# Optimization experiments

Hardware: AMD Instinct MI355X
Metric: run time of the kernel (lower is better)

Reference implementation:

```python
import jax, jax.numpy as jnp
import numpy as np

# dims
B, T, HID = 2, 2048, 2048
HK, HV, DK, DV, KW = 16, 32, 128, 128, 4
KEY_DIM = HK * DK          # 2048
VAL_DIM = HV * DV          # 4096
CONV_DIM = 2 * KEY_DIM + VAL_DIM  # 8192
EPS = 1e-6


def setup_inputs() -> dict:
    key = jax.random.key(0)
    ks = jax.random.split(key, 10)
    s = 0.02
    return {
        "x": jax.random.normal(ks[0], (B, T, HID), jnp.float32),
        "input_pos": jnp.arange(T, dtype=jnp.int64),
        "W_qkv": jax.random.normal(ks[1], (CONV_DIM, HID), jnp.float32) * s,
        "W_z": jax.random.normal(ks[2], (VAL_DIM, HID), jnp.float32) * s,
        "W_b": jax.random.normal(ks[3], (HV, HID), jnp.float32) * s,
        "W_a": jax.random.normal(ks[4], (HV, HID), jnp.float32) * s,
        "conv_w": jax.random.normal(ks[5], (CONV_DIM, 1, KW), jnp.float32) * 0.2,
        "dt_bias": jnp.ones((HV,), jnp.float32),
        "A_log": jnp.log(jax.random.uniform(ks[6], (HV,), jnp.float32, 1e-3, 16.0)),
        "norm_weight": jnp.ones((DV,), jnp.float32),
        "W_out": jax.random.normal(ks[7], (HID, VAL_DIM), jnp.float32) * s,
    }


def _l2norm(t):
    n = jnp.sqrt(jnp.sum(t * t, axis=-1, keepdims=True))
    return t / jnp.maximum(n, 1e-12)


def _gdn_scan(q, k, v, g, beta):
    # per-batch: q,k [T,HV,DK], v [T,HV,DV], g,beta [T,HV]
    scale = DK ** -0.5
    def step(S, inp):  # S: [HV, DK, DV]
        qt, kt, vt, gt, bt = inp
        S = S * jnp.exp(gt)[:, None, None]
        kv = jnp.einsum('hk,hkv->hv', kt, S)
        S = S + jnp.einsum('hk,hv->hkv', kt, bt[:, None] * (vt - kv))
        o = jnp.einsum('hk,hkv->hv', qt * scale, S)
        return S, o
    S0 = jnp.zeros((HV, DK, DV), q.dtype)
    _, o = jax.lax.scan(step, S0, (q, k, v, g, beta))
    return o  # [T, HV, DV]


def reference(x, input_pos, W_qkv, W_z, W_b, W_a, conv_w, dt_bias, A_log, norm_weight, W_out):
    # conv_state / recurrent_state buffers start at zero (and input_pos[0]==0 resets them),
    # so the causal conv reduces to left-padded depthwise conv and the scan starts from S=0.
    mixed_qkv = jnp.einsum('bth,ch->btc', x, W_qkv)                    # [B,T,CONV_DIM]
    z = jnp.einsum('bth,vh->btv', x, W_z).reshape(B, T, HV, DV)
    beta = jax.nn.sigmoid(jnp.einsum('bth,nh->btn', x, W_b))           # [B,T,HV]
    a = jnp.einsum('bth,nh->btn', x, W_a)
    g = -jnp.exp(A_log) * jax.nn.softplus(a + dt_bias)                 # [B,T,HV]

    # causal depthwise conv1d over time
    xc = mixed_qkv.transpose(0, 2, 1)                                  # [B,C,T]
    yc = jax.lax.conv_general_dilated(
        xc, conv_w, window_strides=(1,), padding=[(KW - 1, 0)],
        dimension_numbers=('NCH', 'OIH', 'NCH'), feature_group_count=CONV_DIM)
    qkv = jax.nn.silu(yc).transpose(0, 2, 1)                           # [B,T,C]

    q = qkv[..., :KEY_DIM].reshape(B, T, HK, DK)
    k = qkv[..., KEY_DIM:2 * KEY_DIM].reshape(B, T, HK, DK)
    v = qkv[..., 2 * KEY_DIM:].reshape(B, T, HV, DV)
    q = _l2norm(q)
    k = _l2norm(k)
    rep = HV // HK
    q = jnp.repeat(q, rep, axis=2)                                     # [B,T,HV,DK]
    k = jnp.repeat(k, rep, axis=2)

    o = jax.vmap(_gdn_scan)(q, k, v, g, beta)                          # [B,T,HV,DV]

    # gated RMSNorm: RMSNorm(o) * weight * silu(z)
    of = o.astype(jnp.float32)
    normed = of * jax.lax.rsqrt(jnp.mean(of * of, axis=-1, keepdims=True) + EPS)
    out = (norm_weight * normed) * jax.nn.silu(z.astype(jnp.float32))
    out = out.reshape(B, T, VAL_DIM)
    return jnp.einsum('btv,hv->bth', out, W_out)
```

## Files before the change

### kernel.cpp

```cpp
#include <hip/hip_runtime.h>

#define BB 2
#define TT 2048
#define HID 2048
#define HK 16
#define HV 32
#define DK 128
#define DV 128
#define KW 4
#define KEY_DIM 2048
#define VAL_DIM 4096
#define CONV_DIM 8192
#define N1PAD 12544
#define M_ROWS 4096
#define CC 64

typedef __attribute__((ext_vector_type(8))) short short8;
typedef __attribute__((ext_vector_type(8))) unsigned short ushort8;
typedef __attribute__((ext_vector_type(4))) float f32x4;

__device__ __forceinline__ unsigned short f2bf(float f) {
  union { float f; unsigned int u; } v; v.f = f;
  unsigned int r = v.u + 0x7FFFu + ((v.u >> 16) & 1u);
  return (unsigned short)(r >> 16);
}
__device__ __forceinline__ float bf2f(unsigned short u) {
  union { unsigned int u; float f; } v; v.u = ((unsigned int)u) << 16; return v.f;
}

template <int CTRL>
__device__ __forceinline__ float dpp_add(float v) {
  union { float f; int i; } a, b;
  a.f = v;
  b.i = __builtin_amdgcn_update_dpp(0, a.i, CTRL, 0xf, 0xf, true);
  return a.f + b.f;
}
template <int CTRL>
__device__ __forceinline__ int dpp_mov(int v) {
  return __builtin_amdgcn_update_dpp(0, v, CTRL, 0xf, 0xf, true);
}
__device__ __forceinline__ float row16_sum(float v) {
  v = dpp_add<0xB1>(v); v = dpp_add<0x4E>(v);
  v = dpp_add<0x141>(v); v = dpp_add<0x140>(v);
  return v;
}
__device__ __forceinline__ float row8_sum(float v) {
  v = dpp_add<0xB1>(v); v = dpp_add<0x4E>(v); v = dpp_add<0x141>(v);
  return v;
}

__device__ __forceinline__ void gload_lds16(const unsigned short* g, unsigned short* l) {
  __builtin_amdgcn_global_load_lds((const __attribute__((address_space(1))) unsigned int*)g,
                                   (__attribute__((address_space(3))) unsigned int*)l,
                                   16, 0, 0);
}
__device__ __forceinline__ void gload_lds4(const float* g, unsigned short* l) {
  __builtin_amdgcn_global_load_lds((const __attribute__((address_space(1))) unsigned int*)g,
                                   (__attribute__((address_space(3))) unsigned int*)l,
                                   4, 0, 0);
}

__device__ __forceinline__ short8 ldswz8(const char* base, int row, int e16) {
  int L = (row << 8) + (e16 << 1);
  return *(const short8*)(base + (L ^ ((row & 7) << 4)));
}
__device__ __forceinline__ short8 ldswz7(const char* base, int row, int e16) {
  int L = (row << 7) + (e16 << 1);
  return *(const short8*)(base + (L ^ ((row & 7) << 4)));
}

__global__ void cvt_bf16(const float* __restrict__ in, unsigned short* __restrict__ out) {
  long i = ((long)blockIdx.x * 256 + threadIdx.x) * 4;
  float4 v = *(const float4*)&in[i];
  unsigned long long p = (unsigned long long)f2bf(v.x)
                       | ((unsigned long long)f2bf(v.y) << 16)
                       | ((unsigned long long)f2bf(v.z) << 32)
                       | ((unsigned long long)f2bf(v.w) << 48);
  *(unsigned long long*)&out[i] = p;
}

__global__ void build_wcat(const float* __restrict__ wqkv, const float* __restrict__ wz,
                           const float* __restrict__ wb, const float* __restrict__ wa,
                           unsigned short* __restrict__ wcat) {
  long idx = (long)blockIdx.x * 256 + threadIdx.x;
  long e = idx * 4;
  long r = e >> 11;
  int cc = (int)(e & 2047);
  unsigned long long p = 0ULL;
  if (r < 12352) {
    const float* src;
    if (r < 8192)       src = wqkv + r * 2048;
    else if (r < 12288) src = wz + (r - 8192) * 2048;
    else if (r < 12320) src = wb + (r - 12288) * 2048;
    else                src = wa + (r - 12320) * 2048;
    float4 v = *(const float4*)&src[cc];
    p = (unsigned long long)f2bf(v.x)
      | ((unsigned long long)f2bf(v.y) << 16)
      | ((unsigned long long)f2bf(v.z) << 32)
      | ((unsigned long long)f2bf(v.w) << 48);
  }
  *(unsigned long long*)&wcat[e] = p;
}

__device__ __forceinline__ void stage256(const unsigned short* __restrict__ G, long rb, int K,
                                         int kt, char* region, int r, int tid, int wid) {
  int i = r * 512 + tid;
  int row = i >> 3;
  int D = i << 4;
  int eb = (D ^ ((row & 7) << 4)) & 127;
  const unsigned short* src = G + (rb + row) * (long)K + kt * 64 + (eb >> 1);
  gload_lds16(src, (unsigned short*)region + r * 4096 + wid * 512);
}

__global__ __launch_bounds__(512, 2) void gemm256(const unsigned short* __restrict__ A,
                                                  const unsigned short* __restrict__ Bw,
                                                  unsigned short* __restrict__ Cout,
                                                  int N, int K) {
  extern __shared__ char gs[];
  const int tid = threadIdx.x, wid = tid >> 6, lane = tid & 63;
  const int lr = lane & 15, lq = lane >> 4;
  const long m0 = (long)blockIdx.y << 8;
  const long n0 = (long)blockIdx.x << 8;
  const int wr = wid >> 2, wc = wid & 3;
  const int nkt = K >> 6;

  f32x4 acc[8][4] = {};

#pragma unroll
  for (int r = 0; r < 4; ++r) {
    stage256(A, m0, K, 0, gs, r, tid, wid);
    stage256(Bw, n0, K, 0, gs + 32768, r, tid, wid);
  }
  asm volatile("s_waitcnt vmcnt(0)" ::: "memory");
  __syncthreads();

  for (int kt = 0; kt < nkt; ++kt) {
    char* cur = gs + ((kt & 1) << 16);
    char* nxt = gs + (((kt + 1) & 1) << 16);
    const char* cA = cur;
    const char* cB = cur + 32768;
    const bool pf = (kt + 1 < nkt);
    short8 bf[2][4];
#pragma unroll
    for (int p = 0; p < 4; ++p) {
      if (pf) {
        stage256(A, m0, K, kt + 1, nxt, p, tid, wid);
        stage256(Bw, n0, K, kt + 1, nxt + 32768, p, tid, wid);
      }
      if (p == 0) {
#pragma unroll
        for (int ks = 0; ks < 2; ++ks)
#pragma unroll
          for (int cf = 0; cf < 4; ++cf)
            bf[ks][cf] = ldswz7(cB, wc * 64 + cf * 16 + lr, ks * 32 + lq * 8);
      }
      short8 af[2][2];
#pragma unroll
      for (int ks = 0; ks < 2; ++ks)
#pragma unroll
        for (int rr = 0; rr < 2; ++rr)
          af[ks][rr] = ldswz7(cA, wr * 128 + (p * 2 + rr) * 16 + lr, ks * 32 + lq * 8);
      __builtin_amdgcn_s_setprio(1);
#pragma unroll
      for (int ks = 0; ks < 2; ++ks)
#pragma unroll
        for (int rr = 0; rr < 2; ++rr)
#pragma unroll
          for (int cf = 0; cf < 4; ++cf)
            acc[p * 2 + rr][cf] = __builtin_amdgcn_mfma_f32_16x16x32_bf16(
                af[ks][rr], bf[ks][cf], acc[p * 2 + rr][cf], 0, 0, 0);
      __builtin_amdgcn_s_setprio(0);
    }
    asm volatile("s_waitcnt vmcnt(0)" ::: "memory");
    __syncthreads();
  }

  const long rbase = m0 + wr * 128 + lq * 4;
  const long cbase = n0 + wc * 64 + lr;
#pragma unroll
  for (int rf = 0; rf < 8; ++rf)
#pragma unroll
    for (int cf = 0; cf < 4; ++cf)
#pragma unroll
      for (int j = 0; j < 4; ++j)
        Cout[(rbase + rf * 16 + j) * N + cbase + cf * 16] = f2bf(acc[rf][cf][j]);
}

template <bool BF16OUT>
__global__ __launch_bounds__(256) void gemm_bt(const unsigned short* __restrict__ A,
                                               const unsigned short* __restrict__ Bw,
                                               void* __restrict__ Cout,
                                               int N, int K) {
  __shared__ unsigned short lds[8192];
  const int tid = threadIdx.x;
  const int wid = tid >> 6;
  const int lane = tid & 63;
  const int m0 = blockIdx.y << 7;
  const int n0 = blockIdx.x << 7;
  const int wr = wid >> 1, wc = wid & 1;

  f32x4 acc[4][4] = {};

  const int srow = (wid << 4) + (lane >> 2);
  const int scol = (lane & 3) << 3;
  const unsigned short* gA0 = A + (long)(m0 + srow) * K + scol;
  const unsigned short* gA1 = A + (long)(m0 + 64 + srow) * K + scol;
  const unsigned short* gB0 = Bw + (long)(n0 + srow) * K + scol;
  const unsigned short* gB1 = Bw + (long)(n0 + 64 + srow) * K + scol;
  unsigned short* ldsA = &lds[wid << 9];
  unsigned short* ldsB = &lds[4096 + (wid << 9)];

  const int lrow = lane & 15;
  const int lk = (lane >> 4) << 3;

  for (int k0 = 0; k0 < K; k0 += 32) {
    __syncthreads();
    gload_lds16(gA0 + k0, ldsA);
    gload_lds16(gA1 + k0, ldsA + 2048);
    gload_lds16(gB0 + k0, ldsB);
    gload_lds16(gB1 + k0, ldsB + 2048);
    __syncthreads();
    short8 av[4], bv[4];
#pragma unroll
    for (int i = 0; i < 4; ++i) {
      av[i] = *(const short8*)&lds[((wr << 6) + (i << 4) + lrow) * 32 + lk];
      bv[i] = *(const short8*)&lds[4096 + ((wc << 6) + (i << 4) + lrow) * 32 + lk];
    }
#pragma unroll
    for (int i = 0; i < 4; ++i)
#pragma unroll
      for (int j = 0; j < 4; ++j)
        acc[i][j] = __builtin_amdgcn_mfma_f32_16x16x32_bf16(av[i], bv[j], acc[i][j], 0, 0, 0);
  }
  const int rbase = m0 + (wr << 6) + ((lane >> 4) << 2);
  const int cbase = n0 + (wc << 6) + (lane & 15);
#pragma unroll
  for (int i = 0; i < 4; ++i)
#pragma unroll
    for (int j = 0; j < 4; ++j)
#pragma unroll
      for (int r = 0; r < 4; ++r) {
        long idx = (long)(rbase + (i << 4) + r) * N + cbase + (j << 4);
        if (BF16OUT) ((unsigned short*)Cout)[idx] = f2bf(acc[i][j][r]);
        else         ((float*)Cout)[idx] = acc[i][j][r];
      }
}

__global__ __launch_bounds__(256) void conv_silu(const unsigned short* __restrict__ C1,
                                                 const float* __restrict__ convw,
                                                 unsigned short* __restrict__ qb,
                                                 unsigned short* __restrict__ kb,
                                                 unsigned short* __restrict__ vb) {
  const int bid = blockIdx.x;
  const int cb = bid & 3, tblk = (bid >> 2) & 63, b = bid >> 8;
  const int c0 = cb * 2048 + threadIdx.x * 8;
  float w0[8], w1[8], w2[8], w3[8];
#pragma unroll
  for (int j = 0; j < 8; ++j) {
    float4 wv = *(const float4*)&convw[(c0 + j) * 4];
    w0[j] = wv.x; w1[j] = wv.y; w2[j] = wv.z; w3[j] = wv.w;
  }
  const int t0 = tblk * 32;
  const long rowbase = ((long)b * TT) * N1PAD + c0;
  float x0[8], x1[8], x2[8];
#pragma unroll
  for (int j = 0; j < 8; ++j) { x0[j] = 0.f; x1[j] = 0.f; x2[j] = 0.f; }
  if (t0 >= 1) { ushort8 r = *(const ushort8*)&C1[rowbase + (long)(t0 - 1) * N1PAD];
#pragma unroll
    for (int j = 0; j < 8; ++j) x2[j] = bf2f(r[j]); }
  if (t0 >= 2) { ushort8 r = *(const ushort8*)&C1[rowbase + (long)(t0 - 2) * N1PAD];
#pragma unroll
    for (int j = 0; j < 8; ++j) x1[j] = bf2f(r[j]); }
  if (t0 >= 3) { ushort8 r = *(const ushort8*)&C1[rowbase + (long)(t0 - 3) * N1PAD];
#pragma unroll
    for (int j = 0; j < 8; ++j) x0[j] = bf2f(r[j]); }

  const float nsc = (cb == 0) ? 0.08838834764831845f : 1.0f;
  for (int t = t0; t < t0 + 32; ++t) {
    ushort8 rr = *(const ushort8*)&C1[rowbase + (long)t * N1PAD];
    float ys[8];
#pragma unroll
    for (int j = 0; j < 8; ++j) {
      float x3 = bf2f(rr[j]);
      float y = w0[j] * x0[j] + w1[j] * x1[j] + w2[j] * x2[j] + w3[j] * x3;
      ys[j] = y / (1.f + __expf(-y));
      x0[j] = x1[j]; x1[j] = x2[j]; x2[j] = x3;
    }
    if (cb < 2) {
      float ss = 0.f;
#pragma unroll
      for (int j = 0; j < 8; ++j) ss = fmaf(ys[j], ys[j], ss);
      ss = row16_sum(ss);
      float sc = nsc / fmaxf(sqrtf(ss), 1e-12f);
#pragma unroll
      for (int j = 0; j < 8; ++j) ys[j] *= sc;
    }
    ushort8 outp;
#pragma unroll
    for (int j = 0; j < 8; ++j) outp[j] = f2bf(ys[j]);
    long m = (long)b * TT + t;
    if (cb == 0)      *(ushort8*)&qb[m * 2048 + threadIdx.x * 8] = outp;
    else if (cb == 1) *(ushort8*)&kb[m * 2048 + threadIdx.x * 8] = outp;
    else              *(ushort8*)&vb[m * 4096 + (cb - 2) * 2048 + threadIdx.x * 8] = outp;
  }
}

__global__ void gbeta(const unsigned short* __restrict__ C1, const float* __restrict__ Alog,
                      const float* __restrict__ dtb, float* __restrict__ graw, float* __restrict__ betab) {
  int idx = blockIdx.x * 256 + threadIdx.x;
  int m = idx >> 5, h = idx & 31;
  float a = bf2f(C1[(long)m * N1PAD + 12320 + h]);
  float bl = bf2f(C1[(long)m * N1PAD + 12288 + h]);
  float xsp = a + dtb[h];
  float sp = (xsp > 20.f) ? xsp : log1pf(expf(xsp));
  graw[idx] = -expf(Alog[h]) * sp;
  betab[idx] = 1.f / (1.f + expf(-bl));
}

#define OFF_K   0
#define OFF_Q   16384
#define OFF_V   32768
#define OFF_G   36864
#define OFF_B2  37120
#define INSZ    37376
#define OFF_KT  74752
#define OFF_SH  91136
#define OFF_SL  99328
#define OFF_A2  107520
#define OFF_MM  124928
#define OFF_BT  133120
#define OFF_BT2 137216
#define OFF_X   141312
#define OFF_CS  149760
#define OFF_EXC 150016
#define OFF_ECT 150272
#define SMEM_SZ 150528

__global__ __launch_bounds__(256) void chunk_scan(const unsigned short* __restrict__ qb,
                                                  const unsigned short* __restrict__ kb,
                                                  const unsigned short* __restrict__ vb,
                                                  const float* __restrict__ graw,
                                                  const float* __restrict__ betab,
                                                  unsigned short* __restrict__ ob) {
  extern __shared__ char smem[];
  const int w = blockIdx.x;
  const int rdec = w >> 5, gdec = w & 31;
  const int bat = gdec >> 4, hk = gdec & 15;
  const int h = hk * 2 + (rdec >> 2), vc = rdec & 3;
  const int tid = threadIdx.x, wid = tid >> 6, lane = tid & 63;
  const int lr = lane & 15, lq = lane >> 4;

  const long kqoff = ((long)bat * TT) * 2048 + hk * 128;
  const long voff  = ((long)bat * TT) * 4096 + h * 128 + vc * 32;
  const long goff  = ((long)bat * TT) * 32 + h;

  f32x4 Smast[4] = {};

  auto stagec = [&](char* inb2, int t0c) {
#pragma unroll
    for (int it = 0; it < 4; ++it) {
      int i = it * 256 + tid;
      int rowk = i >> 4;
      int L = (i << 4) ^ ((rowk & 7) << 4);
      int srcoff = (L & 255) >> 1;
      long grow = (long)(t0c + rowk) * 2048 + srcoff;
      gload_lds16(kb + kqoff + grow, (unsigned short*)(inb2 + OFF_K) + it * 2048 + wid * 512);
      gload_lds16(qb + kqoff + grow, (unsigned short*)(inb2 + OFF_Q) + it * 2048 + wid * 512);
    }
    {
      int i = tid;
      gload_lds16(vb + voff + (long)(t0c + (i >> 2)) * 4096 + (i & 3) * 8,
                  (unsigned short*)(inb2 + OFF_V) + wid * 512);
    }
    if (wid == 3) gload_lds4(graw  + goff + (long)(t0c + lane) * 32, (unsigned short*)(inb2 + OFF_G));
    if (wid == 2) gload_lds4(betab + goff + (long)(t0c + lane) * 32, (unsigned short*)(inb2 + OFF_B2));
  };

  stagec(smem, 0);
#pragma unroll
  for (int z = 0; z < 4; ++z)
    *(f32x4*)(smem + OFF_SH + tid * 64 + z * 16) = (f32x4){0.f, 0.f, 0.f, 0.f};
  asm volatile("s_waitcnt vmcnt(0)" ::: "memory");
  __syncthreads();

  for (int ct = 0; ct < TT / CC; ++ct) {
    char* inb = smem + (ct & 1) * INSZ;
    if (ct + 1 < TT / CC) stagec(smem + ((ct + 1) & 1) * INSZ, (ct + 1) * CC);
    if (wid == 0) {
      float gv = ((const float*)(inb + OFF_G))[lane];
#pragma unroll
      for (int off = 1; off < 64; off <<= 1) {
        float n = __shfl_up(gv, off);
        if (lane >= off) gv += n;
      }
      ((float*)(smem + OFF_CS))[lane] = gv;
      ((float*)(smem + OFF_EXC))[lane] = __expf(gv);
      float tot = __shfl(gv, 63);
      ((float*)(smem + OFF_ECT))[lane] = __expf(tot - gv);
    } else {
      int bt_ = tid - 64;
#pragma unroll
      for (int it = 0; it < 3; ++it) {
        int idx = it * 192 + bt_;
        if (idx < 512) {
          int tp = idx & 31, dkb = idx >> 5;
          short8 r0 = ldswz8(inb + OFF_K, 2 * tp, dkb * 8);
          short8 r1 = ldswz8(inb + OFF_K, 2 * tp + 1, dkb * 8);
#pragma unroll
          for (int e = 0; e < 8; ++e) {
            int dk = dkb * 8 + e;
            unsigned int pk = (unsigned int)(unsigned short)r0[e]
                            | ((unsigned int)(unsigned short)r1[e] << 16);
            int Lk = (dk << 7) + (tp << 2);
            *(unsigned int*)(smem + OFF_KT + (Lk ^ ((dk & 7) << 4))) = pk;
          }
        }
      }
    }
    __syncthreads();

    f32x4 aKK[4] = {}, aQK[4] = {}, aKS[2] = {}, aQS[2] = {};
    float oq[8];
#pragma unroll
    for (int kk = 0; kk < 4; ++kk) {
      int ke = kk * 32 + lq * 8;
      short8 avk = ldswz8(inb + OFF_K, 16 * wid + lr, ke);
      short8 avq = ldswz8(inb + OFF_Q, 16 * wid + lr, ke);
#pragma unroll
      for (int tc = 0; tc < 4; ++tc) {
        short8 bvk = ldswz8(inb + OFF_K, 16 * tc + lr, ke);
        aKK[tc] = __builtin_amdgcn_mfma_f32_16x16x32_bf16(avk, bvk, aKK[tc], 0, 0, 0);
        aQK[tc] = __builtin_amdgcn_mfma_f32_16x16x32_bf16(avq, bvk, aQK[tc], 0, 0, 0);
      }
      short8 bH0 = ldswz8(smem + OFF_SH, lr, ke);
      short8 bH1 = ldswz8(smem + OFF_SH, 16 + lr, ke);
      short8 bL0 = ldswz8(smem + OFF_SL, lr, ke);
      short8 bL1 = ldswz8(smem + OFF_SL, 16 + lr, ke);
      aKS[0] = __builtin_amdgcn_mfma_f32_16x16x32_bf16(avk, bH0, aKS[0], 0, 0, 0);
      aKS[0] = __builtin_amdgcn_mfma_f32_16x16x32_bf16(avk, bL0, aKS[0], 0, 0, 0);
      aKS[1] = __builtin_amdgcn_mfma_f32_16x16x32_bf16(avk, bH1, aKS[1], 0, 0, 0);
      aKS[1] = __builtin_amdgcn_mfma_f32_16x16x32_bf16(avk, bL1, aKS[1], 0, 0, 0);
      aQS[0] = __builtin_amdgcn_mfma_f32_16x16x32_bf16(avq, bH0, aQS[0], 0, 0, 0);
      aQS[0] = __builtin_amdgcn_mfma_f32_16x16x32_bf16(avq, bL0, aQS[0], 0, 0, 0);
      aQS[1] = __builtin_amdgcn_mfma_f32_16x16x32_bf16(avq, bH1, aQS[1], 0, 0, 0);
      aQS[1] = __builtin_amdgcn_mfma_f32_16x16x32_bf16(avq, bL1, aQS[1], 0, 0, 0);
    }
    {
      const float* csp  = (const float*)(smem + OFF_CS);
      const float* excp = (const float*)(smem + OFF_EXC);
      const float* betp = (const float*)(inb + OFF_B2);
      const unsigned short* vp = (const unsigned short*)(inb + OFF_V);
      float cst[4], bt4[4], ext[4];
#pragma unroll
      for (int j = 0; j < 4; ++j) {
        int t = 16 * wid + lq * 4 + j;
        cst[j] = csp[t]; bt4[j] = betp[t]; ext[j] = excp[t];
      }
#pragma unroll
      for (int tc = 0; tc < 4; ++tc) {
        int i = 16 * tc + lr;
        float csi = csp[i];
#pragma unroll
        for (int j = 0; j < 4; ++j) {
          int t = 16 * wid + lq * 4 + j;
          float e = __expf(cst[j] - csi);
          float av = (i < t) ? bt4[j] * e * aKK[tc][j] : 0.f;
          ((float*)(smem + OFF_A2))[t * 68 + (i & 7) * 8 + (i >> 3)] = av;
          float mv = (i <= t) ? e * aQK[tc][j] : 0.f;
          unsigned int mvb = f2bf(mv);
          unsigned int mvp = (unsigned int)dpp_mov<0xB1>((int)mvb);
          if (!(lr & 1)) {
            int Lm = (t << 7) + (i << 1);
            *(unsigned int*)(smem + OFF_MM + (Lm ^ ((t & 7) << 4))) = mvb | (mvp << 16);
          }
        }
      }
#pragma unroll
      for (int nt = 0; nt < 2; ++nt) {
        int vcl = nt * 16 + lr;
#pragma unroll
        for (int j = 0; j < 4; ++j) {
          int t = 16 * wid + lq * 4 + j;
          float vvv = bf2f(vp[t * 32 + vcl]);
          float x = bt4[j] * (vvv - ext[j] * aKS[nt][j]);
          ((float*)(smem + OFF_X))[t * 33 + vcl] = x;
          oq[nt * 4 + j] = ext[j] * aQS[nt][j];
        }
      }
    }
    __syncthreads();

    {
      const float* A2p  = (const float*)(smem + OFF_A2);
      const float* Xp   = (const float*)(smem + OFF_X);
      const float* ectp = (const float*)(smem + OFF_ECT);
      const int col = tid >> 3, rr = tid & 7;
      float bbv[8] = {0.f, 0.f, 0.f, 0.f, 0.f, 0.f, 0.f, 0.f};
#pragma unroll
      for (int t = 0; t < 64; ++t) {
        float4 a0 = *(const float4*)(A2p + t * 68 + rr * 8);
        float4 a1 = *(const float4*)(A2p + t * 68 + rr * 8 + 4);
        float sA = fmaf(a0.y, bbv[1], a0.x * bbv[0]);
        sA = fmaf(a0.z, bbv[2], sA); sA = fmaf(a0.w, bbv[3], sA);
        float sB = fmaf(a1.y, bbv[5], a1.x * bbv[4]);
        sB = fmaf(a1.z, bbv[6], sB); sB = fmaf(a1.w, bbv[7], sB);
        float s = row8_sum(sA + sB);
        float btv = Xp[t * 33 + col] - s;
        if (rr == (t & 7)) bbv[t >> 3] = btv;
      }
#pragma unroll
      for (int k = 0; k < 8; ++k) {
        int t = 8 * k + rr;
        int Lb = (col << 7) + (t << 1);
        int Pb = Lb ^ ((col & 7) << 4);
        *(unsigned short*)(smem + OFF_BT + Pb)  = f2bf(bbv[k]);
        *(unsigned short*)(smem + OFF_BT2 + Pb) = f2bf(bbv[k] * ectp[t]);
      }
    }
    __syncthreads();

    {
      f32x4 accO[2];
#pragma unroll
      for (int nt = 0; nt < 2; ++nt)
        accO[nt] = (f32x4){oq[nt * 4 + 0], oq[nt * 4 + 1], oq[nt * 4 + 2], oq[nt * 4 + 3]};
#pragma unroll
      for (int kk2 = 0; kk2 < 2; ++kk2) {
        int ke = kk2 * 32 + lq * 8;
        short8 aM = ldswz7(smem + OFF_MM, 16 * wid + lr, ke);
#pragma unroll
        for (int nt = 0; nt < 2; ++nt) {
          short8 bB = ldswz7(smem + OFF_BT, 16 * nt + lr, ke);
          accO[nt] = __builtin_amdgcn_mfma_f32_16x16x32_bf16(aM, bB, accO[nt], 0, 0, 0);
        }
      }
#pragma unroll
      for (int nt = 0; nt < 2; ++nt)
#pragma unroll
        for (int j = 0; j < 4; ++j) {
          int t = 16 * wid + lq * 4 + j;
          int vcl = nt * 16 + lr;
          long tg = (long)(bat * TT + ct * CC + t);
          ob[(tg * 32 + h) * 128 + vc * 32 + vcl] = f2bf(accO[nt][j]);
        }

      int mr = wid & 1, nc0 = (wid >> 1) * 4;
      f32x4 accP[4] = {};
#pragma unroll
      for (int kk2 = 0; kk2 < 2; ++kk2) {
        int ke = kk2 * 32 + lq * 8;
        short8 aB2 = ldswz7(smem + OFF_BT2, 16 * mr + lr, ke);
#pragma unroll
        for (int c4 = 0; c4 < 4; ++c4) {
          short8 bK = ldswz7(smem + OFF_KT, 16 * (nc0 + c4) + lr, ke);
          accP[c4] = __builtin_amdgcn_mfma_f32_16x16x32_bf16(aB2, bK, accP[c4], 0, 0, 0);
        }
      }
      float ecC = ((const float*)(smem + OFF_EXC))[63];
#pragma unroll
      for (int c4 = 0; c4 < 4; ++c4)
#pragma unroll
        for (int j = 0; j < 4; ++j) {
          float sv = fmaf(ecC, Smast[c4][j], accP[c4][j]);
          Smast[c4][j] = sv;
          int vcr = 16 * mr + lq * 4 + j;
          int dk  = 16 * (nc0 + c4) + lr;
          unsigned int hi = f2bf(sv);
          unsigned int lo = f2bf(sv - bf2f((unsigned short)hi));
          unsigned int hip = (unsigned int)dpp_mov<0xB1>((int)hi);
          unsigned int lop = (unsigned int)dpp_mov<0xB1>((int)lo);
          if (!(lr & 1)) {
            int Ls = (vcr << 8) + (dk << 1);
            int Ps = Ls ^ ((vcr & 7) << 4);
            *(unsigned int*)(smem + OFF_SH + Ps) = hi | (hip << 16);
            *(unsigned int*)(smem + OFF_SL + Ps) = lo | (lop << 16);
          }
        }
    }
    asm volatile("s_waitcnt vmcnt(0)" ::: "memory");
    __syncthreads();
  }
}

__global__ __launch_bounds__(256) void norm_silu(const unsigned short* __restrict__ ob,
                                                 const unsigned short* __restrict__ C1,
                                                 const float* __restrict__ nw,
                                                 unsigned short* __restrict__ nrm) {
  int unit = blockIdx.x * 4 + (threadIdx.x >> 6);
  int lane = threadIdx.x & 63;
  int m = unit >> 5, h = unit & 31;
  unsigned int uo = *(const unsigned int*)&ob[(long)unit * 128 + lane * 2];
  float o0 = bf2f((unsigned short)(uo & 0xffff));
  float o1 = bf2f((unsigned short)(uo >> 16));
  float ss = o0 * o0 + o1 * o1;
#pragma unroll
  for (int mm = 1; mm < 64; mm <<= 1) ss += __shfl_xor(ss, mm);
  float rs = rsqrtf(ss * (1.0f / 128.0f) + 1e-6f);
  unsigned int uz = *(const unsigned int*)&C1[(long)m * N1PAD + 8192 + h * 128 + lane * 2];
  float z0 = bf2f((unsigned short)(uz & 0xffff));
  float z1 = bf2f((unsigned short)(uz >> 16));
  float s0 = z0 / (1.f + expf(-z0));
  float s1 = z1 / (1.f + expf(-z1));
  float r0 = o0 * rs * nw[lane * 2] * s0;
  float r1 = o1 * rs * nw[lane * 2 + 1] * s1;
  unsigned int pk = (unsigned int)f2bf(r0) | ((unsigned int)f2bf(r1) << 16);
  *(unsigned int*)&nrm[(long)unit * 128 + lane * 2] = pk;
}

extern "C" void kernel_launch(void* const* d_in, const int* in_sizes, int n_in,
                              void* d_out, int out_size, void* d_ws, size_t ws_size,
                              hipStream_t stream) {
  const float* x    = (const float*)d_in[0];
  const float* Wqkv = (const float*)d_in[2];
  const float* Wz   = (const float*)d_in[3];
  const float* Wb   = (const float*)d_in[4];
  const float* Wa   = (const float*)d_in[5];
  const float* convw= (const float*)d_in[6];
  const float* dtb  = (const float*)d_in[7];
  const float* Alog = (const float*)d_in[8];
  const float* nw   = (const float*)d_in[9];
  const float* Wout = (const float*)d_in[10];
  float* out = (float*)d_out;

  char* ws = (char*)d_ws;
  const size_t OFF_C1    = 0;
  const size_t OFF_XB    = 102760448;
  const size_t OFF_WCAT  = 119537664;
  const size_t OFF_QB    = OFF_XB;
  const size_t OFF_KB    = 119537664;
  const size_t OFF_VB    = 136314880;
  const size_t OFF_EG    = 170917888;
  const size_t OFF_BE    = 171442176;
  const size_t OFF_OB    = 171966464;
  const size_t OFF_NRM   = OFF_QB;
  const size_t OFF_WOUTB = OFF_VB;

  unsigned short* C1    = (unsigned short*)(ws + OFF_C1);
  unsigned short* xb    = (unsigned short*)(ws + OFF_XB);
  unsigned short* wcat  = (unsigned short*)(ws + OFF_WCAT);
  unsigned short* qbuf  = (unsigned short*)(ws + OFF_QB);
  unsigned short* kbuf  = (unsigned short*)(ws + OFF_KB);
  unsigned short* vbuf  = (unsigned short*)(ws + OFF_VB);
  float*          egb   = (float*)(ws + OFF_EG);
  float*          betab = (float*)(ws + OFF_BE);
  unsigned short* obuf  = (unsigned short*)(ws + OFF_OB);
  unsigned short* nrm   = (unsigned short*)(ws + OFF_NRM);
  unsigned short* woutb = (unsigned short*)(ws + OFF_WOUTB);
  (void)ws_size; (void)in_sizes; (void)n_in; (void)out_size;

  static int smem_set = 0;
  if (!smem_set) {
    hipFuncSetAttribute(reinterpret_cast<const void*>(chunk_scan),
                        hipFuncAttributeMaxDynamicSharedMemorySize, SMEM_SZ);
    hipFuncSetAttribute(reinterpret_cast<const void*>(gemm256),
                        hipFuncAttributeMaxDynamicSharedMemorySize, 131072);
    smem_set = 1;
  }

  cvt_bf16<<<8192, 256, 0, stream>>>(x, xb);
  build_wcat<<<25088, 256, 0, stream>>>(Wqkv, Wz, Wb, Wa, wcat);
  gemm256<<<dim3(N1PAD / 256, M_ROWS / 256), 512, 131072, stream>>>(xb, wcat, C1, N1PAD, 2048);
  conv_silu<<<512, 256, 0, stream>>>(C1, convw, qbuf, kbuf, vbuf);
  gbeta<<<512, 256, 0, stream>>>(C1, Alog, dtb, egb, betab);
  chunk_scan<<<256, 256, SMEM_SZ, stream>>>(qbuf, kbuf, vbuf, egb, betab, obuf);
  cvt_bf16<<<8192, 256, 0, stream>>>(Wout, woutb);
  norm_silu<<<32768, 256, 0, stream>>>(obuf, C1, nw, nrm);
  gemm_bt<false><<<dim3(2048 / 128, M_ROWS / 128), 256, 0, stream>>>(nrm, woutb, out, 2048, 4096);
}
```

Baseline: 848.1 us.

## Double chunk_scan wavefronts per block, load Q into registers, single-buffer LDS

The chunk_scan block grows from 256 to 512 threads, and the MFMA work per chunk is split so each wave handles half the tiles. Q is no longer staged in LDS. It is loaded straight into registers and prefetched one chunk ahead. The LDS double buffer is replaced by a single buffer whose next-chunk staging is done by the idle upper four waves while waves 0-3 do the triangular solve, which shrinks shared memory from about 150KB to 97KB. The aim is to hide the latency of the serial per-chunk recurrence with more waves per CU. The cost is less overlap of loads, since staging now sits between barriers, and more global load traffic for Q.

```diff
diff --git a/kernel.cpp b/kernel.cpp
--- a/kernel.cpp
+++ b/kernel.cpp
@@ -318,30 +318,28 @@
 }
 
 #define OFF_K   0
-#define OFF_Q   16384
-#define OFF_V   32768
-#define OFF_G   36864
-#define OFF_B2  37120
-#define INSZ    37376
-#define OFF_KT  74752
-#define OFF_SH  91136
-#define OFF_SL  99328
-#define OFF_A2  107520
-#define OFF_MM  124928
-#define OFF_BT  133120
-#define OFF_BT2 137216
-#define OFF_X   141312
-#define OFF_CS  149760
-#define OFF_EXC 150016
-#define OFF_ECT 150272
-#define SMEM_SZ 150528
-
-__global__ __launch_bounds__(256) void chunk_scan(const unsigned short* __restrict__ qb,
-                                                  const unsigned short* __restrict__ kb,
-                                                  const unsigned short* __restrict__ vb,
-                                                  const float* __restrict__ graw,
-                                                  const float* __restrict__ betab,
-                                                  unsigned short* __restrict__ ob) {
+#define OFF_V   16384
+#define OFF_G   20480
+#define OFF_B2  20736
+#define OFF_KT  20992
+#define OFF_SH  37376
+#define OFF_SL  45568
+#define OFF_A2  53760
+#define OFF_MM  71168
+#define OFF_BT  79360
+#define OFF_BT2 83456
+#define OFF_X   87552
+#define OFF_CS  96000
+#define OFF_EXC 96256
+#define OFF_ECT 96512
+#define SMEM_SZ 96768
+
+__global__ __launch_bounds__(512, 2) void chunk_scan(const unsigned short* __restrict__ qb,
+                                                     const unsigned short* __restrict__ kb,
+                                                     const unsigned short* __restrict__ vb,
+                                                     const float* __restrict__ graw,
+                                                     const float* __restrict__ betab,
+                                                     unsigned short* __restrict__ ob) {
   extern __shared__ char smem[];
   const int w = blockIdx.x;
   const int rdec = w >> 5, gdec = w & 31;
@@ -349,45 +347,67 @@
   const int h = hk * 2 + (rdec >> 2), vc = rdec & 3;
   const int tid = threadIdx.x, wid = tid >> 6, lane = tid & 63;
   const int lr = lane & 15, lq = lane >> 4;
+  const int rg = wid & 3, half = wid >> 2;
+  const int mr = wid & 1, nc2 = (wid >> 1) & 3;
 
   const long kqoff = ((long)bat * TT) * 2048 + hk * 128;
   const long voff  = ((long)bat * TT) * 4096 + h * 128 + vc * 32;
   const long goff  = ((long)bat * TT) * 32 + h;
 
-  f32x4 Smast[4] = {};
-
-  auto stagec = [&](char* inb2, int t0c) {
+  f32x4 Smast[2] = {};
+
+  auto stage_full = [&](int t0c) {
+#pragma unroll
+    for (int it = 0; it < 2; ++it) {
+      int i = it * 512 + tid;
+      int row = i >> 4;
+      int L = ((i & 15) << 4) ^ ((row & 7) << 4);
+      long grow = (long)(t0c + row) * 2048 + (L >> 1);
+      gload_lds16(kb + kqoff + grow, (unsigned short*)(smem + OFF_K) + it * 4096 + wid * 512);
+    }
+    if (tid < 256)
+      gload_lds16(vb + voff + (long)(t0c + (tid >> 2)) * 4096 + (tid & 3) * 8,
+                  (unsigned short*)(smem + OFF_V) + wid * 512);
+    if (wid == 6) gload_lds4(graw  + goff + (long)(t0c + lane) * 32, (unsigned short*)(smem + OFF_G));
+    if (wid == 7) gload_lds4(betab + goff + (long)(t0c + lane) * 32, (unsigned short*)(smem + OFF_B2));
+  };
+  auto stage_part = [&](int t0c) {
+    int tid2 = tid - 256, wid2 = wid - 4;
 #pragma unroll
     for (int it = 0; it < 4; ++it) {
-      int i = it * 256 + tid;
-      int rowk = i >> 4;
-      int L = (i << 4) ^ ((rowk & 7) << 4);
-      int srcoff = (L & 255) >> 1;
-      long grow = (long)(t0c + rowk) * 2048 + srcoff;
-      gload_lds16(kb + kqoff + grow, (unsigned short*)(inb2 + OFF_K) + it * 2048 + wid * 512);
-      gload_lds16(qb + kqoff + grow, (unsigned short*)(inb2 + OFF_Q) + it * 2048 + wid * 512);
-    }
+      int i = it * 256 + tid2;
+      int row = i >> 4;
+      int L = ((i & 15) << 4) ^ ((row & 7) << 4);
+      long grow = (long)(t0c + row) * 2048 + (L >> 1);
+      gload_lds16(kb + kqoff + grow, (unsigned short*)(smem + OFF_K) + it * 2048 + wid2 * 512);
+    }
+    gload_lds16(vb + voff + (long)(t0c + (tid2 >> 2)) * 4096 + (tid2 & 3) * 8,
+                (unsigned short*)(smem + OFF_V) + wid2 * 512);
+    if (wid == 4) gload_lds4(graw  + goff + (long)(t0c + lane) * 32, (unsigned short*)(smem + OFF_G));
+    if (wid == 5) gload_lds4(betab + goff + (long)(t0c + lane) * 32, (unsigned short*)(smem + OFF_B2));
+  };
+  auto loadQ = [&](short8 (&qr)[4], int t0c) {
+#pragma unroll
+    for (int kk = 0; kk < 4; ++kk)
+      qr[kk] = *(const short8*)&qb[kqoff + (long)(t0c + 16 * rg + lr) * 2048 + kk * 32 + lq * 8];
+  };
+
+  auto body = [&](int ct, short8 (&qcur)[4], short8 (&qnext)[4]) {
     {
-      int i = tid;
-      gload_lds16(vb + voff + (long)(t0c + (i >> 2)) * 4096 + (i & 3) * 8,
-                  (unsigned short*)(inb2 + OFF_V) + wid * 512);
-    }
-    if (wid == 3) gload_lds4(graw  + goff + (long)(t0c + lane) * 32, (unsigned short*)(inb2 + OFF_G));
-    if (wid == 2) gload_lds4(betab + goff + (long)(t0c + lane) * 32, (unsigned short*)(inb2 + OFF_B2));
-  };
-
-  stagec(smem, 0);
-#pragma unroll
-  for (int z = 0; z < 4; ++z)
-    *(f32x4*)(smem + OFF_SH + tid * 64 + z * 16) = (f32x4){0.f, 0.f, 0.f, 0.f};
-  asm volatile("s_waitcnt vmcnt(0)" ::: "memory");
-  __syncthreads();
-
-  for (int ct = 0; ct < TT / CC; ++ct) {
-    char* inb = smem + (ct & 1) * INSZ;
-    if (ct + 1 < TT / CC) stagec(smem + ((ct + 1) & 1) * INSZ, (ct + 1) * CC);
+      int tp = tid & 31, dkb = tid >> 5;
+      short8 r0 = ldswz8(smem + OFF_K, 2 * tp, dkb * 8);
+      short8 r1 = ldswz8(smem + OFF_K, 2 * tp + 1, dkb * 8);
+#pragma unroll
+      for (int e = 0; e < 8; ++e) {
+        int dk = dkb * 8 + e;
+        unsigned int pk = (unsigned int)(unsigned short)r0[e]
+                        | ((unsigned int)(unsigned short)r1[e] << 16);
+        int Lk = (dk << 7) + (tp << 2);
+        *(unsigned int*)(smem + OFF_KT + (Lk ^ ((dk & 7) << 4))) = pk;
+      }
+    }
     if (wid == 0) {
-      float gv = ((const float*)(inb + OFF_G))[lane];
+      float gv = ((const float*)(smem + OFF_G))[lane];
 #pragma unroll
       for (int off = 1; off < 64; off <<= 1) {
         float n = __shfl_up(gv, off);
@@ -397,76 +417,51 @@
       ((float*)(smem + OFF_EXC))[lane] = __expf(gv);
       float tot = __shfl(gv, 63);
       ((float*)(smem + OFF_ECT))[lane] = __expf(tot - gv);
-    } else {
-      int bt_ = tid - 64;
-#pragma unroll
-      for (int it = 0; it < 3; ++it) {
-        int idx = it * 192 + bt_;
-        if (idx < 512) {
-          int tp = idx & 31, dkb = idx >> 5;
-          short8 r0 = ldswz8(inb + OFF_K, 2 * tp, dkb * 8);
-          short8 r1 = ldswz8(inb + OFF_K, 2 * tp + 1, dkb * 8);
-#pragma unroll
-          for (int e = 0; e < 8; ++e) {
-            int dk = dkb * 8 + e;
-            unsigned int pk = (unsigned int)(unsigned short)r0[e]
-                            | ((unsigned int)(unsigned short)r1[e] << 16);
-            int Lk = (dk << 7) + (tp << 2);
-            *(unsigned int*)(smem + OFF_KT + (Lk ^ ((dk & 7) << 4))) = pk;
-          }
-        }
-      }
     }
     __syncthreads();
 
-    f32x4 aKK[4] = {}, aQK[4] = {}, aKS[2] = {}, aQS[2] = {};
-    float oq[8];
+    f32x4 aKK[2] = {}, aQK[2] = {}, aKS = {}, aQS = {};
+    float oq[4];
 #pragma unroll
     for (int kk = 0; kk < 4; ++kk) {
       int ke = kk * 32 + lq * 8;
-      short8 avk = ldswz8(inb + OFF_K, 16 * wid + lr, ke);
-      short8 avq = ldswz8(inb + OFF_Q, 16 * wid + lr, ke);
-#pragma unroll
-      for (int tc = 0; tc < 4; ++tc) {
-        short8 bvk = ldswz8(inb + OFF_K, 16 * tc + lr, ke);
-        aKK[tc] = __builtin_amdgcn_mfma_f32_16x16x32_bf16(avk, bvk, aKK[tc], 0, 0, 0);
-        aQK[tc] = __builtin_amdgcn_mfma_f32_16x16x32_bf16(avq, bvk, aQK[tc], 0, 0, 0);
-      }
-      short8 bH0 = ldswz8(smem + OFF_SH, lr, ke);
-      short8 bH1 = ldswz8(smem + OFF_SH, 16 + lr, ke);
-      short8 bL0 = ldswz8(smem + OFF_SL, lr, ke);
-      short8 bL1 = ldswz8(smem + OFF_SL, 16 + lr, ke);
-      aKS[0] = __builtin_amdgcn_mfma_f32_16x16x32_bf16(avk, bH0, aKS[0], 0, 0, 0);
-      aKS[0] = __builtin_amdgcn_mfma_f32_16x16x32_bf16(avk, bL0, aKS[0], 0, 0, 0);
-      aKS[1] = __builtin_amdgcn_mfma_f32_16x16x32_bf16(avk, bH1, aKS[1], 0, 0, 0);
-      aKS[1] = __builtin_amdgcn_mfma_f32_16x16x32_bf16(avk, bL1, aKS[1], 0, 0, 0);
-      aQS[0] = __builtin_amdgcn_mfma_f32_16x16x32_bf16(avq, bH0, aQS[0], 0, 0, 0);
-      aQS[0] = __builtin_amdgcn_mfma_f32_16x16x32_bf16(avq, bL0, aQS[0], 0, 0, 0);
-      aQS[1] = __builtin_amdgcn_mfma_f32_16x16x32_bf16(avq, bH1, aQS[1], 0, 0, 0);
-      aQS[1] = __builtin_amdgcn_mfma_f32_16x16x32_bf16(avq, bL1, aQS[1], 0, 0, 0);
+      short8 avk = ldswz8(smem + OFF_K, 16 * rg + lr, ke);
+      short8 avq = qcur[kk];
+#pragma unroll
+      for (int tc2 = 0; tc2 < 2; ++tc2) {
+        short8 bvk = ldswz8(smem + OFF_K, 16 * (2 * half + tc2) + lr, ke);
+        aKK[tc2] = __builtin_amdgcn_mfma_f32_16x16x32_bf16(avk, bvk, aKK[tc2], 0, 0, 0);
+        aQK[tc2] = __builtin_amdgcn_mfma_f32_16x16x32_bf16(avq, bvk, aQK[tc2], 0, 0, 0);
+      }
+      short8 bH = ldswz8(smem + OFF_SH, 16 * half + lr, ke);
+      short8 bL = ldswz8(smem + OFF_SL, 16 * half + lr, ke);
+      aKS = __builtin_amdgcn_mfma_f32_16x16x32_bf16(avk, bH, aKS, 0, 0, 0);
+      aKS = __builtin_amdgcn_mfma_f32_16x16x32_bf16(avk, bL, aKS, 0, 0, 0);
+      aQS = __builtin_amdgcn_mfma_f32_16x16x32_bf16(avq, bH, aQS, 0, 0, 0);
+      aQS = __builtin_amdgcn_mfma_f32_16x16x32_bf16(avq, bL, aQS, 0, 0, 0);
     }
     {
       const float* csp  = (const float*)(smem + OFF_CS);
       const float* excp = (const float*)(smem + OFF_EXC);
-      const float* betp = (const float*)(inb + OFF_B2);
-      const unsigned short* vp = (const unsigned short*)(inb + OFF_V);
+      const float* betp = (const float*)(smem + OFF_B2);
+      const unsigned short* vp = (const unsigned short*)(smem + OFF_V);
       float cst[4], bt4[4], ext[4];
 #pragma unroll
       for (int j = 0; j < 4; ++j) {
-        int t = 16 * wid + lq * 4 + j;
+        int t = 16 * rg + lq * 4 + j;
         cst[j] = csp[t]; bt4[j] = betp[t]; ext[j] = excp[t];
       }
 #pragma unroll
-      for (int tc = 0; tc < 4; ++tc) {
-        int i = 16 * tc + lr;
+      for (int tc2 = 0; tc2 < 2; ++tc2) {
+        int i = 16 * (2 * half + tc2) + lr;
         float csi = csp[i];
 #pragma unroll
         for (int j = 0; j < 4; ++j) {
-          int t = 16 * wid + lq * 4 + j;
+          int t = 16 * rg + lq * 4 + j;
           float e = __expf(cst[j] - csi);
-          float av = (i < t) ? bt4[j] * e * aKK[tc][j] : 0.f;
+          float av = (i < t) ? bt4[j] * e * aKK[tc2][j] : 0.f;
           ((float*)(smem + OFF_A2))[t * 68 + (i & 7) * 8 + (i >> 3)] = av;
-          float mv = (i <= t) ? e * aQK[tc][j] : 0.f;
+          float mv = (i <= t) ? e * aQK[tc2][j] : 0.f;
           unsigned int mvb = f2bf(mv);
           unsigned int mvp = (unsigned int)dpp_mov<0xB1>((int)mvb);
           if (!(lr & 1)) {
@@ -475,22 +470,20 @@
           }
         }
       }
-#pragma unroll
-      for (int nt = 0; nt < 2; ++nt) {
-        int vcl = nt * 16 + lr;
-#pragma unroll
-        for (int j = 0; j < 4; ++j) {
-          int t = 16 * wid + lq * 4 + j;
-          float vvv = bf2f(vp[t * 32 + vcl]);
-          float x = bt4[j] * (vvv - ext[j] * aKS[nt][j]);
-          ((float*)(smem + OFF_X))[t * 33 + vcl] = x;
-          oq[nt * 4 + j] = ext[j] * aQS[nt][j];
-        }
+      int vcl = 16 * half + lr;
+#pragma unroll
+      for (int j = 0; j < 4; ++j) {
+        int t = 16 * rg + lq * 4 + j;
+        float vvv = bf2f(vp[t * 32 + vcl]);
+        float x = bt4[j] * (vvv - ext[j] * aKS[j]);
+        ((float*)(smem + OFF_X))[t * 33 + vcl] = x;
+        oq[j] = ext[j] * aQS[j];
       }
     }
     __syncthreads();
 
-    {
+    if (ct + 1 < TT / CC) loadQ(qnext, (ct + 1) * CC);
+    if (wid < 4) {
       const float* A2p  = (const float*)(smem + OFF_A2);
       const float* Xp   = (const float*)(smem + OFF_X);
       const float* ectp = (const float*)(smem + OFF_ECT);
@@ -516,55 +509,48 @@
         *(unsigned short*)(smem + OFF_BT + Pb)  = f2bf(bbv[k]);
         *(unsigned short*)(smem + OFF_BT2 + Pb) = f2bf(bbv[k] * ectp[t]);
       }
+    } else if (ct + 1 < TT / CC) {
+      stage_part((ct + 1) * CC);
     }
     __syncthreads();
 
     {
-      f32x4 accO[2];
-#pragma unroll
-      for (int nt = 0; nt < 2; ++nt)
-        accO[nt] = (f32x4){oq[nt * 4 + 0], oq[nt * 4 + 1], oq[nt * 4 + 2], oq[nt * 4 + 3]};
+      f32x4 accO = (f32x4){oq[0], oq[1], oq[2], oq[3]};
 #pragma unroll
       for (int kk2 = 0; kk2 < 2; ++kk2) {
         int ke = kk2 * 32 + lq * 8;
-        short8 aM = ldswz7(smem + OFF_MM, 16 * wid + lr, ke);
-#pragma unroll
-        for (int nt = 0; nt < 2; ++nt) {
-          short8 bB = ldswz7(smem + OFF_BT, 16 * nt + lr, ke);
-          accO[nt] = __builtin_amdgcn_mfma_f32_16x16x32_bf16(aM, bB, accO[nt], 0, 0, 0);
-        }
-      }
-#pragma unroll
-      for (int nt = 0; nt < 2; ++nt)
-#pragma unroll
-        for (int j = 0; j < 4; ++j) {
-          int t = 16 * wid + lq * 4 + j;
-          int vcl = nt * 16 + lr;
-          long tg = (long)(bat * TT + ct * CC + t);
-          ob[(tg * 32 + h) * 128 + vc * 32 + vcl] = f2bf(accO[nt][j]);
-        }
-
-      int mr = wid & 1, nc0 = (wid >> 1) * 4;
-      f32x4 accP[4] = {};
+        short8 aM = ldswz7(smem + OFF_MM, 16 * rg + lr, ke);
+        short8 bB = ldswz7(smem + OFF_BT, 16 * half + lr, ke);
+        accO = __builtin_amdgcn_mfma_f32_16x16x32_bf16(aM, bB, accO, 0, 0, 0);
+      }
+      int vcl = 16 * half + lr;
+#pragma unroll
+      for (int j = 0; j < 4; ++j) {
+        int t = 16 * rg + lq * 4 + j;
+        long tg = (long)(bat * TT + ct * CC + t);
+        ob[(tg * 32 + h) * 128 + vc * 32 + vcl] = f2bf(accO[j]);
+      }
+
+      f32x4 accP[2] = {};
 #pragma unroll
       for (int kk2 = 0; kk2 < 2; ++kk2) {
         int ke = kk2 * 32 + lq * 8;
         short8 aB2 = ldswz7(smem + OFF_BT2, 16 * mr + lr, ke);
 #pragma unroll
-        for (int c4 = 0; c4 < 4; ++c4) {
-          short8 bK = ldswz7(smem + OFF_KT, 16 * (nc0 + c4) + lr, ke);
+        for (int c4 = 0; c4 < 2; ++c4) {
+          short8 bK = ldswz7(smem + OFF_KT, 16 * (2 * nc2 + c4) + lr, ke);
           accP[c4] = __builtin_amdgcn_mfma_f32_16x16x32_bf16(aB2, bK, accP[c4], 0, 0, 0);
         }
       }
       float ecC = ((const float*)(smem + OFF_EXC))[63];
 #pragma unroll
-      for (int c4 = 0; c4 < 4; ++c4)
+      for (int c4 = 0; c4 < 2; ++c4)
 #pragma unroll
         for (int j = 0; j < 4; ++j) {
           float sv = fmaf(ecC, Smast[c4][j], accP[c4][j]);
           Smast[c4][j] = sv;
           int vcr = 16 * mr + lq * 4 + j;
-          int dk  = 16 * (nc0 + c4) + lr;
+          int dk  = 16 * (2 * nc2 + c4) + lr;
           unsigned int hi = f2bf(sv);
           unsigned int lo = f2bf(sv - bf2f((unsigned short)hi));
           unsigned int hip = (unsigned int)dpp_mov<0xB1>((int)hi);
@@ -579,6 +565,19 @@
     }
     asm volatile("s_waitcnt vmcnt(0)" ::: "memory");
     __syncthreads();
+  };
+
+  short8 qA[4], qB[4];
+  loadQ(qA, 0);
+  stage_full(0);
+  *(f32x4*)(smem + OFF_SH + tid * 32)      = (f32x4){0.f, 0.f, 0.f, 0.f};
+  *(f32x4*)(smem + OFF_SH + tid * 32 + 16) = (f32x4){0.f, 0.f, 0.f, 0.f};
+  asm volatile("s_waitcnt vmcnt(0)" ::: "memory");
+  __syncthreads();
+
+  for (int cp = 0; cp < TT / CC / 2; ++cp) {
+    body(2 * cp, qA, qB);
+    body(2 * cp + 1, qB, qA);
   }
 }
 
@@ -662,7 +661,7 @@
   gemm256<<<dim3(N1PAD / 256, M_ROWS / 256), 512, 131072, stream>>>(xb, wcat, C1, N1PAD, 2048);
   conv_silu<<<512, 256, 0, stream>>>(C1, convw, qbuf, kbuf, vbuf);
   gbeta<<<512, 256, 0, stream>>>(C1, Alog, dtb, egb, betab);
-  chunk_scan<<<256, 256, SMEM_SZ, stream>>>(qbuf, kbuf, vbuf, egb, betab, obuf);
+  chunk_scan<<<256, 512, SMEM_SZ, stream>>>(qbuf, kbuf, vbuf, egb, betab, obuf);
   cvt_bf16<<<8192, 256, 0, stream>>>(Wout, woutb);
   norm_silu<<<32768, 256, 0, stream>>>(obuf, C1, nw, nrm);
   gemm_bt<false><<<dim3(2048 / 128, M_ROWS / 128), 256, 0, stream>>>(nrm, woutb, out, 2048, 4096);
```

New measurement: 784.0 us. -7.6%, faster.
